# Optimization experiments

Hardware: AMD Instinct MI355X
Metric: run time of the kernel (lower is better)

Reference implementation:

```python
import jax, jax.numpy as jnp
import numpy as np

SIZES = [384, 160, 128, 96, 1]   # aev_length followed by hidden sizes (ANI-1 config)
N_SPECIES = 4                    # H, C, N, O
N_LAYERS = 4
CELU_ALPHA = 0.1
B, A = 128, 512                  # molecules, atoms per molecule


def setup_inputs() -> dict:
    key = jax.random.key(0)
    ks = jax.random.split(key, 2 + 2 * N_LAYERS)
    inp = {
        "fullaev": jax.random.normal(ks[0], (B, A, SIZES[0]), dtype=jnp.float32),
        "species": jax.random.randint(ks[1], (A,), 0, N_SPECIES, dtype=jnp.int32),
    }
    # Per-species stacked Linear params, torch default init: U(-1/sqrt(fan_in), 1/sqrt(fan_in))
    for l in range(N_LAYERS):
        bound = 1.0 / np.sqrt(SIZES[l])
        inp[f"W{l}"] = jax.random.uniform(ks[2 + 2 * l], (N_SPECIES, SIZES[l + 1], SIZES[l]),
                                          dtype=jnp.float32, minval=-bound, maxval=bound)
        inp[f"b{l}"] = jax.random.uniform(ks[3 + 2 * l], (N_SPECIES, SIZES[l + 1]),
                                          dtype=jnp.float32, minval=-bound, maxval=bound)
    return inp


def reference(fullaev, species, W0, b0, W1, b1, W2, b2, W3, b3):
    # fullaev: [B, A, aev_len]; species: [A] int route ids.
    # Equivalent to the per-atom Python loop: each atom goes through its
    # species' MLP; gather the per-atom weight matrices and do one batched GEMM per layer.
    Ws = (W0, W1, W2, W3)
    bs = (b0, b1, b2, b3)
    y = fullaev
    for l in range(N_LAYERS):
        Wa = Ws[l][species]          # [A, out, in] gathered per atom
        ba = bs[l][species]          # [A, out]
        y = jnp.einsum('bai,aoi->bao', y, Wa) + ba[None, :, :]
        if l < N_LAYERS - 1:
            y = jax.nn.celu(y, alpha=CELU_ALPHA)
    # stack over atoms + sum reducer over atom dim, then squeeze -> [B]
    return jnp.squeeze(jnp.sum(y, axis=1), axis=-1)
```

## Files before the change

kernel.cpp:

```cpp
#include <hip/hip_runtime.h>
#include <hip/hip_bf16.h>


typedef float f32x4 __attribute__((ext_vector_type(4)));
typedef short s16x8 __attribute__((ext_vector_type(8)));

#define NMOL   128
#define NATOM  512
#define AEV    384
#define MT     64
#define XLD    392
#define Y0LD   168
#define Y1LD   136
#define Y2LD   104

#define Y1_OFF 10752
#define RED_OFF 19456

#define PL0    61440
#define PL1    20480
#define PL2    12288
#define BASE0  0
#define BASE1  245760
#define BASE2  327680
#define WP_BYTE_OFF 262144

__device__ __forceinline__ ushort f2bf(float f) {
    uint u = __float_as_uint(f);
    return (ushort)((u + 0x7fffu + ((u >> 16) & 1u)) >> 16);
}
__device__ __forceinline__ float bf2f(ushort h) {
    return __uint_as_float(((uint)h) << 16);
}
__device__ __forceinline__ float celu_f(float v) {
    return fmaxf(v, 0.0f) + fminf(0.1f * (__expf(10.0f * v) - 1.0f), 0.0f);
}
__device__ __forceinline__ uint pk2bf(float x, float y) {
    __hip_bfloat162 h2;
    h2.x = __float2bfloat16(x);
    h2.y = __float2bfloat16(y);
    return *(uint*)&h2;
}

__global__ __launch_bounds__(256) void prep_kernel(
    const float* __restrict__ W0, const float* __restrict__ W1,
    const float* __restrict__ W2, ushort* __restrict__ Wp)
{
    const int idx = blockIdx.x * 256 + threadIdx.x;
    int n, k0, KS;
    size_t base;
    const float* src;
    if (idx < 30720) {
        const int s = idx / 7680, r = idx % 7680;
        n = r / 48; k0 = (r % 48) * 8; KS = 12;
        src = W0 + (size_t)idx * 8;
        base = BASE0 + (size_t)s * PL0;
    } else if (idx < 40960) {
        const int i2 = idx - 30720;
        const int s = i2 / 2560, r = i2 % 2560;
        n = r / 20; k0 = (r % 20) * 8; KS = 5;
        src = W1 + (size_t)i2 * 8;
        base = BASE1 + (size_t)s * PL1;
    } else {
        const int i2 = idx - 40960;
        const int s = i2 / 1536, r = i2 % 1536;
        n = r / 16; k0 = (r % 16) * 8; KS = 4;
        src = W2 + (size_t)i2 * 8;
        base = BASE2 + (size_t)s * PL2;
    }
    const float4 v0 = *(const float4*)(src);
    const float4 v1 = *(const float4*)(src + 4);
    const size_t fo = (size_t)((((n >> 4) * KS + (k0 >> 5)) * 64
                                + ((k0 & 31) >> 3) * 16 + (n & 15)) * 8);
    uint4 w;
    w.x = pk2bf(v0.x, v0.y);
    w.y = pk2bf(v0.z, v0.w);
    w.z = pk2bf(v1.x, v1.y);
    w.w = pk2bf(v1.z, v1.w);
    *(uint4*)(Wp + base + fo) = w;
}

__global__ __attribute__((amdgpu_flat_work_group_size(512, 512),
                          amdgpu_waves_per_eu(6, 6)))
void ani_mfma_kernel(
    const float* __restrict__ aev, const int* __restrict__ species,
    const ushort* __restrict__ Wp,
    const float* __restrict__ b0, const float* __restrict__ b1,
    const float* __restrict__ b2,
    const float* __restrict__ W3, const float* __restrict__ b3,
    float* __restrict__ partial)
{
    __shared__ __align__(16) ushort smem[MT * XLD];

    const int bid  = blockIdx.x;
    const int a    = bid >> 1;
    const int half = bid & 1;
    const int tid  = threadIdx.x;
    const int lane = tid & 63;
    const int wid  = tid >> 6;
    const int mgrp = wid >> 2;
    const int ngrp = wid & 3;
    const bool has3 = (ngrp < 2);

    const int s = species[a];
    const ushort* Bh0 = Wp + BASE0 + (size_t)s * PL0;
    const ushort* Bh1 = Wp + BASE1 + (size_t)s * PL1;
    const ushort* Bh2 = Wp + BASE2 + (size_t)s * PL2;
    const float* b0s = b0 + s * 160;
    const float* b1s = b1 + s * 128;
    const float* b2s = b2 + s * 96;
    const float* w3s = W3 + s * 96;
    const float  bb3 = b3[s];

    ushort* X     = smem;
    ushort* y0buf = smem;
    ushort* y1buf = smem + Y1_OFF;
    ushort* y2buf = smem;

    const f32x4 zero = {0.f, 0.f, 0.f, 0.f};

    {
        const int srow = tid >> 3;
        const int scol = tid & 7;
        const float* sp = aev + ((size_t)(half * MT + srow) * NATOM + a) * AEV
                          + scol * 8;
        float4 rv[12];
        #pragma unroll
        for (int jp = 0; jp < 6; ++jp) {
            rv[2 * jp]     = *(const float4*)(sp + jp * 64);
            rv[2 * jp + 1] = *(const float4*)(sp + jp * 64 + 4);
        }
        ushort* xd = X + srow * XLD + scol * 8;
        #pragma unroll
        for (int jp = 0; jp < 6; ++jp) {
            uint4 w;
            w.x = pk2bf(rv[2 * jp].x,     rv[2 * jp].y);
            w.y = pk2bf(rv[2 * jp].z,     rv[2 * jp].w);
            w.z = pk2bf(rv[2 * jp + 1].x, rv[2 * jp + 1].y);
            w.w = pk2bf(rv[2 * jp + 1].z, rv[2 * jp + 1].w);
            *(uint4*)(xd + jp * 64) = w;
        }
    }
    __syncthreads();

    f32x4 acc[2][3];
    #pragma unroll
    for (int mf = 0; mf < 2; ++mf)
        #pragma unroll
        for (int ti = 0; ti < 3; ++ti) acc[mf][ti] = zero;
    {
        const ushort* arow0 = X + (mgrp * 32 + (lane & 15)) * XLD + (lane >> 4) * 8;
        #pragma unroll
        for (int gks = 0; gks < 12; ++gks) {
            s16x8 ah[2];
            ah[0] = *(const s16x8*)(arow0 + gks * 32);
            ah[1] = *(const s16x8*)(arow0 + 16 * XLD + gks * 32);
            const s16x8 bh0 = *(const s16x8*)(
                Bh0 + ((size_t)((ngrp    ) * 12 + gks) * 64 + lane) * 8);
            const s16x8 bh1 = *(const s16x8*)(
                Bh0 + ((size_t)((ngrp + 4) * 12 + gks) * 64 + lane) * 8);
            acc[0][0] = __builtin_amdgcn_mfma_f32_16x16x32_bf16(ah[0], bh0, acc[0][0], 0, 0, 0);
            acc[1][0] = __builtin_amdgcn_mfma_f32_16x16x32_bf16(ah[1], bh0, acc[1][0], 0, 0, 0);
            acc[0][1] = __builtin_amdgcn_mfma_f32_16x16x32_bf16(ah[0], bh1, acc[0][1], 0, 0, 0);
            acc[1][1] = __builtin_amdgcn_mfma_f32_16x16x32_bf16(ah[1], bh1, acc[1][1], 0, 0, 0);
            if (has3) {
                const s16x8 bh2 = *(const s16x8*)(
                    Bh0 + ((size_t)((ngrp + 8) * 12 + gks) * 64 + lane) * 8);
                acc[0][2] = __builtin_amdgcn_mfma_f32_16x16x32_bf16(ah[0], bh2, acc[0][2], 0, 0, 0);
                acc[1][2] = __builtin_amdgcn_mfma_f32_16x16x32_bf16(ah[1], bh2, acc[1][2], 0, 0, 0);
            }
        }
    }
    __syncthreads();

    #pragma unroll
    for (int ti = 0; ti < 3; ++ti) {
        if (ti < 2 || has3) {
            const int n = (ngrp + 4 * ti) * 16 + (lane & 15);
            const float bv = b0s[n];
            #pragma unroll
            for (int mf = 0; mf < 2; ++mf) {
                #pragma unroll
                for (int r = 0; r < 4; ++r) {
                    const int row = mgrp * 32 + mf * 16 + (lane >> 4) * 4 + r;
                    y0buf[row * Y0LD + n] = f2bf(celu_f(acc[mf][ti][r] + bv));
                }
            }
        }
    }
    __syncthreads();

    f32x4 acc1[2][2];
    #pragma unroll
    for (int mf = 0; mf < 2; ++mf) { acc1[mf][0] = zero; acc1[mf][1] = zero; }
    {
        const ushort* arow0 = y0buf + (mgrp * 32 + (lane & 15)) * Y0LD + (lane >> 4) * 8;
        #pragma unroll
        for (int ks = 0; ks < 5; ++ks) {
            s16x8 ah[2];
            ah[0] = *(const s16x8*)(arow0 + ks * 32);
            ah[1] = *(const s16x8*)(arow0 + 16 * Y0LD + ks * 32);
            const s16x8 bh0 = *(const s16x8*)(
                Bh1 + ((size_t)((ngrp    ) * 5 + ks) * 64 + lane) * 8);
            const s16x8 bh1 = *(const s16x8*)(
                Bh1 + ((size_t)((ngrp + 4) * 5 + ks) * 64 + lane) * 8);
            acc1[0][0] = __builtin_amdgcn_mfma_f32_16x16x32_bf16(ah[0], bh0, acc1[0][0], 0, 0, 0);
            acc1[1][0] = __builtin_amdgcn_mfma_f32_16x16x32_bf16(ah[1], bh0, acc1[1][0], 0, 0, 0);
            acc1[0][1] = __builtin_amdgcn_mfma_f32_16x16x32_bf16(ah[0], bh1, acc1[0][1], 0, 0, 0);
            acc1[1][1] = __builtin_amdgcn_mfma_f32_16x16x32_bf16(ah[1], bh1, acc1[1][1], 0, 0, 0);
        }
    }

    #pragma unroll
    for (int t = 0; t < 2; ++t) {
        const int n = (ngrp + 4 * t) * 16 + (lane & 15);
        const float bv = b1s[n];
        #pragma unroll
        for (int mf = 0; mf < 2; ++mf) {
            #pragma unroll
            for (int r = 0; r < 4; ++r) {
                const int row = mgrp * 32 + mf * 16 + (lane >> 4) * 4 + r;
                y1buf[row * Y1LD + n] = f2bf(celu_f(acc1[mf][t][r] + bv));
            }
        }
    }
    __syncthreads();

    f32x4 acc2[2][2];
    #pragma unroll
    for (int mf = 0; mf < 2; ++mf) { acc2[mf][0] = zero; acc2[mf][1] = zero; }
    {
        const ushort* arow0 = y1buf + (mgrp * 32 + (lane & 15)) * Y1LD + (lane >> 4) * 8;
        #pragma unroll
        for (int ks = 0; ks < 4; ++ks) {
            s16x8 ah[2];
            ah[0] = *(const s16x8*)(arow0 + ks * 32);
            ah[1] = *(const s16x8*)(arow0 + 16 * Y1LD + ks * 32);
            const s16x8 bh0 = *(const s16x8*)(
                Bh2 + ((size_t)((ngrp) * 4 + ks) * 64 + lane) * 8);
            acc2[0][0] = __builtin_amdgcn_mfma_f32_16x16x32_bf16(ah[0], bh0, acc2[0][0], 0, 0, 0);
            acc2[1][0] = __builtin_amdgcn_mfma_f32_16x16x32_bf16(ah[1], bh0, acc2[1][0], 0, 0, 0);
            if (has3) {
                const s16x8 bh1 = *(const s16x8*)(
                    Bh2 + ((size_t)((ngrp + 4) * 4 + ks) * 64 + lane) * 8);
                acc2[0][1] = __builtin_amdgcn_mfma_f32_16x16x32_bf16(ah[0], bh1, acc2[0][1], 0, 0, 0);
                acc2[1][1] = __builtin_amdgcn_mfma_f32_16x16x32_bf16(ah[1], bh1, acc2[1][1], 0, 0, 0);
            }
        }
    }

    #pragma unroll
    for (int t = 0; t < 2; ++t) {
        if (t == 0 || has3) {
            const int n = (ngrp + 4 * t) * 16 + (lane & 15);
            const float bv = b2s[n];
            #pragma unroll
            for (int mf = 0; mf < 2; ++mf) {
                #pragma unroll
                for (int r = 0; r < 4; ++r) {
                    const int row = mgrp * 32 + mf * 16 + (lane >> 4) * 4 + r;
                    y2buf[row * Y2LD + n] = f2bf(celu_f(acc2[mf][t][r] + bv));
                }
            }
        }
    }
    __syncthreads();

    {
        float* red = (float*)(smem + RED_OFF);
        const int m = tid & (MT - 1);
        const int q = tid >> 6;
        float accv = 0.f;
        #pragma unroll
        for (int ii = 0; ii < 12; ++ii) {
            const int i = q * 12 + ii;
            accv = fmaf(w3s[i], bf2f(y2buf[m * Y2LD + i]), accv);
        }
        red[q * MT + m] = accv;
        __syncthreads();
        if (tid < MT) {
            float sm = bb3;
            #pragma unroll
            for (int qq = 0; qq < 8; ++qq) sm += red[qq * MT + tid];
            partial[(size_t)a * NMOL + half * MT + tid] = sm;
        }
    }
}

__global__ __launch_bounds__(256) void reduce_kernel(
    const float* __restrict__ partial, float* __restrict__ out)
{
    __shared__ float red[256];
    const int m = blockIdx.x;
    const int t = threadIdx.x;
    float sv = partial[(size_t)t * NMOL + m] + partial[(size_t)(t + 256) * NMOL + m];
    red[t] = sv;
    __syncthreads();
    #pragma unroll
    for (int w = 128; w > 0; w >>= 1) {
        if (t < w) red[t] += red[t + w];
        __syncthreads();
    }
    if (t == 0) out[m] = red[0];
}

extern "C" void kernel_launch(void* const* d_in, const int* in_sizes, int n_in,
                              void* d_out, int out_size, void* d_ws, size_t ws_size,
                              hipStream_t stream) {
    const float* aev     = (const float*)d_in[0];
    const int*   species = (const int*)  d_in[1];
    const float* W0 = (const float*)d_in[2];
    const float* b0 = (const float*)d_in[3];
    const float* W1 = (const float*)d_in[4];
    const float* b1 = (const float*)d_in[5];
    const float* W2 = (const float*)d_in[6];
    const float* b2 = (const float*)d_in[7];
    const float* W3 = (const float*)d_in[8];
    const float* b3 = (const float*)d_in[9];
    float* out     = (float*)d_out;
    float* partial = (float*)d_ws;
    ushort* Wp     = (ushort*)((char*)d_ws + WP_BYTE_OFF);

    prep_kernel<<<184, 256, 0, stream>>>(W0, W1, W2, Wp);
    ani_mfma_kernel<<<NATOM * 2, 512, 0, stream>>>(aev, species, Wp,
                                                   b0, b1, b2, W3, b3, partial);
    reduce_kernel<<<NMOL, 256, 0, stream>>>(partial, out);
}
```

Baseline: 52.68 us.

## Stream AEV tile into LDS with async global_load_lds double buffering

Replaces the synchronous load-convert-store of the full 64x384 fp32 AEV tile with direct global-to-LDS async loads (global_load_lds) in six K-chunks. The chunks are double-buffered in a swizzled fp32 layout, with bf16 conversion done at fragment read time. Shared memory drops from 64x392 shorts to 20480 shorts, and waves_per_eu rises from 6 to 8 for more occupancy. The aim is to overlap AEV fetch with layer-0 MFMAs, at the cost of one barrier per chunk and repeated conversion work in each wave.

```diff
diff --git a/kernel.cpp b/kernel.cpp
--- a/kernel.cpp
+++ b/kernel.cpp
@@ -9,11 +9,9 @@
 #define NATOM  512
 #define AEV    384
 #define MT     64
-#define XLD    392
 #define Y0LD   168
 #define Y1LD   136
 #define Y2LD   104
-
 #define Y1_OFF 10752
 #define RED_OFF 19456
 
@@ -24,6 +22,9 @@
 #define BASE1  245760
 #define BASE2  327680
 #define WP_BYTE_OFF 262144
+
+typedef const __attribute__((address_space(1))) void* gas_ptr;
+typedef __attribute__((address_space(3))) void* las_ptr;
 
 __device__ __forceinline__ ushort f2bf(float f) {
     uint u = __float_as_uint(f);
@@ -81,7 +82,7 @@
 }
 
 __global__ __attribute__((amdgpu_flat_work_group_size(512, 512),
-                          amdgpu_waves_per_eu(6, 6)))
+                          amdgpu_waves_per_eu(8, 8)))
 void ani_mfma_kernel(
     const float* __restrict__ aev, const int* __restrict__ species,
     const ushort* __restrict__ Wp,
@@ -90,7 +91,7 @@
     const float* __restrict__ W3, const float* __restrict__ b3,
     float* __restrict__ partial)
 {
-    __shared__ __align__(16) ushort smem[MT * XLD];
+    __shared__ __align__(16) ushort smem[20480];
 
     const int bid  = blockIdx.x;
     const int a    = bid >> 1;
@@ -112,66 +113,79 @@
     const float* w3s = W3 + s * 96;
     const float  bb3 = b3[s];
 
-    ushort* X     = smem;
     ushort* y0buf = smem;
     ushort* y1buf = smem + Y1_OFF;
     ushort* y2buf = smem;
 
+    const int mol8 = lane >> 3;
+    const int swz  = (lane & 7) ^ mol8;
+    const char* gsrc = (const char*)(aev
+        + ((size_t)(half * MT + wid * 8 + mol8) * NATOM + a) * AEV) + swz * 16;
+    const int ldsbase = wid * 2048;
+
     const f32x4 zero = {0.f, 0.f, 0.f, 0.f};
+    f32x4 acc[2][3];
+    #pragma unroll
+    for (int mf = 0; mf < 2; ++mf)
+        #pragma unroll
+        for (int ti = 0; ti < 3; ++ti) acc[mf][ti] = zero;
 
     {
-        const int srow = tid >> 3;
-        const int scol = tid & 7;
-        const float* sp = aev + ((size_t)(half * MT + srow) * NATOM + a) * AEV
-                          + scol * 8;
-        float4 rv[12];
-        #pragma unroll
-        for (int jp = 0; jp < 6; ++jp) {
-            rv[2 * jp]     = *(const float4*)(sp + jp * 64);
-            rv[2 * jp + 1] = *(const float4*)(sp + jp * 64 + 4);
-        }
-        ushort* xd = X + srow * XLD + scol * 8;
-        #pragma unroll
-        for (int jp = 0; jp < 6; ++jp) {
-            uint4 w;
-            w.x = pk2bf(rv[2 * jp].x,     rv[2 * jp].y);
-            w.y = pk2bf(rv[2 * jp].z,     rv[2 * jp].w);
-            w.z = pk2bf(rv[2 * jp + 1].x, rv[2 * jp + 1].y);
-            w.w = pk2bf(rv[2 * jp + 1].z, rv[2 * jp + 1].w);
-            *(uint4*)(xd + jp * 64) = w;
-        }
-    }
-    __syncthreads();
-
-    f32x4 acc[2][3];
-    #pragma unroll
-    for (int mf = 0; mf < 2; ++mf)
-        #pragma unroll
-        for (int ti = 0; ti < 3; ++ti) acc[mf][ti] = zero;
-    {
-        const ushort* arow0 = X + (mgrp * 32 + (lane & 15)) * XLD + (lane >> 4) * 8;
-        #pragma unroll
-        for (int gks = 0; gks < 12; ++gks) {
-            s16x8 ah[2];
-            ah[0] = *(const s16x8*)(arow0 + gks * 32);
-            ah[1] = *(const s16x8*)(arow0 + 16 * XLD + gks * 32);
-            const s16x8 bh0 = *(const s16x8*)(
-                Bh0 + ((size_t)((ngrp    ) * 12 + gks) * 64 + lane) * 8);
-            const s16x8 bh1 = *(const s16x8*)(
-                Bh0 + ((size_t)((ngrp + 4) * 12 + gks) * 64 + lane) * 8);
-            acc[0][0] = __builtin_amdgcn_mfma_f32_16x16x32_bf16(ah[0], bh0, acc[0][0], 0, 0, 0);
-            acc[1][0] = __builtin_amdgcn_mfma_f32_16x16x32_bf16(ah[1], bh0, acc[1][0], 0, 0, 0);
-            acc[0][1] = __builtin_amdgcn_mfma_f32_16x16x32_bf16(ah[0], bh1, acc[0][1], 0, 0, 0);
-            acc[1][1] = __builtin_amdgcn_mfma_f32_16x16x32_bf16(ah[1], bh1, acc[1][1], 0, 0, 0);
-            if (has3) {
-                const s16x8 bh2 = *(const s16x8*)(
+        const int r0 = mgrp * 32 + (lane & 15);
+        const int c2 = (lane >> 4) * 2;
+
+        __builtin_amdgcn_global_load_lds((gas_ptr)(gsrc),
+            (las_ptr)((char*)smem + ldsbase), 16, 0, 0);
+        __builtin_amdgcn_global_load_lds((gas_ptr)(gsrc + 128),
+            (las_ptr)((char*)smem + ldsbase + 1024), 16, 0, 0);
+        __syncthreads();
+
+        #pragma unroll
+        for (int t = 0; t < 6; ++t) {
+            if (t < 5) {
+                const char* g = gsrc + (t + 1) * 256;
+                char* d = (char*)smem + ((t + 1) & 1) * 16384 + ldsbase;
+                __builtin_amdgcn_global_load_lds((gas_ptr)(g),       (las_ptr)(d),        16, 0, 0);
+                __builtin_amdgcn_global_load_lds((gas_ptr)(g + 128), (las_ptr)(d + 1024), 16, 0, 0);
+            }
+            const float* Xb = (const float*)((const char*)smem + (t & 1) * 16384);
+            #pragma unroll
+            for (int gs = 0; gs < 2; ++gs) {
+                const int gks = t * 2 + gs;
+                const s16x8 bh0 = *(const s16x8*)(
+                    Bh0 + ((size_t)((ngrp    ) * 12 + gks) * 64 + lane) * 8);
+                const s16x8 bh1 = *(const s16x8*)(
+                    Bh0 + ((size_t)((ngrp + 4) * 12 + gks) * 64 + lane) * 8);
+                s16x8 bh2;
+                if (has3) bh2 = *(const s16x8*)(
                     Bh0 + ((size_t)((ngrp + 8) * 12 + gks) * 64 + lane) * 8);
-                acc[0][2] = __builtin_amdgcn_mfma_f32_16x16x32_bf16(ah[0], bh2, acc[0][2], 0, 0, 0);
-                acc[1][2] = __builtin_amdgcn_mfma_f32_16x16x32_bf16(ah[1], bh2, acc[1][2], 0, 0, 0);
-            }
-        }
-    }
-    __syncthreads();
+
+                s16x8 ah[2];
+                #pragma unroll
+                for (int mf = 0; mf < 2; ++mf) {
+                    const int r = r0 + mf * 16;
+                    const float* rp = Xb + (r >> 3) * 512 + gs * 256 + (r & 7) * 32;
+                    const f32x4 v0 = *(const f32x4*)(rp + (((c2    ) ^ (r & 7)) * 4));
+                    const f32x4 v1 = *(const f32x4*)(rp + (((c2 + 1) ^ (r & 7)) * 4));
+                    union { s16x8 v; uint u[4]; } rr;
+                    rr.u[0] = pk2bf(v0.x, v0.y);
+                    rr.u[1] = pk2bf(v0.z, v0.w);
+                    rr.u[2] = pk2bf(v1.x, v1.y);
+                    rr.u[3] = pk2bf(v1.z, v1.w);
+                    ah[mf] = rr.v;
+                }
+                acc[0][0] = __builtin_amdgcn_mfma_f32_16x16x32_bf16(ah[0], bh0, acc[0][0], 0, 0, 0);
+                acc[1][0] = __builtin_amdgcn_mfma_f32_16x16x32_bf16(ah[1], bh0, acc[1][0], 0, 0, 0);
+                acc[0][1] = __builtin_amdgcn_mfma_f32_16x16x32_bf16(ah[0], bh1, acc[0][1], 0, 0, 0);
+                acc[1][1] = __builtin_amdgcn_mfma_f32_16x16x32_bf16(ah[1], bh1, acc[1][1], 0, 0, 0);
+                if (has3) {
+                    acc[0][2] = __builtin_amdgcn_mfma_f32_16x16x32_bf16(ah[0], bh2, acc[0][2], 0, 0, 0);
+                    acc[1][2] = __builtin_amdgcn_mfma_f32_16x16x32_bf16(ah[1], bh2, acc[1][2], 0, 0, 0);
+                }
+            }
+            __syncthreads();
+        }
+    }
 
     #pragma unroll
     for (int ti = 0; ti < 3; ++ti) {
```

Result: faster. 44.12 us (-16.2%).
